# Kernel tuning notes

Measured on AMD Instinct MI355X. Metric: run time of the kernel, lower is better.

## Reference

```python
import jax, jax.numpy as jnp
import numpy as np

N = 50000
F = 128
E = 800000
HOP = 3
ALPHA = 0.2  # leaky relu slope


def setup_inputs() -> dict:
    key = jax.random.key(0)
    ks = jax.random.split(key, 6)
    x = jax.random.normal(ks[0], (N, F), dtype=jnp.float32)
    h0 = jax.random.normal(ks[1], (N, F), dtype=jnp.float32)
    edge_index = jax.random.randint(ks[2], (2, E), 0, N, dtype=jnp.int32)
    edge_weight = jax.random.uniform(ks[3], (E,), dtype=jnp.float32)
    # xavier-uniform-ish params
    lim_w = float(np.sqrt(6.0 / (F + F)))
    W_att = jax.random.uniform(ks[4], (F, F), dtype=jnp.float32, minval=-lim_w, maxval=lim_w)
    lim_a = 1.414 * float(np.sqrt(6.0 / (2 * F + 1)))
    a = jax.random.uniform(ks[5], (2 * F, 1), dtype=jnp.float32, minval=-lim_a, maxval=lim_a)
    temp = jnp.zeros((4,), dtype=jnp.float32)
    return {"x": x, "h0": h0, "edge_index": edge_index, "edge_weight": edge_weight,
            "W_att": W_att, "a": a, "temp": temp}


def _segment_softmax(e, rows, num_segments):
    m = jax.ops.segment_max(e, rows, num_segments=num_segments)
    m = jnp.where(jnp.isfinite(m), m, 0.0)  # guard empty rows
    ex = jnp.exp(e - m[rows])
    s = jax.ops.segment_sum(ex, rows, num_segments=num_segments)
    s = jnp.where(s > 0, s, 1.0)
    return ex / s[rows]


def reference(x, h0, edge_index, edge_weight, W_att, a, temp):
    rows, cols = edge_index[0], edge_index[1]
    # --- attention (edge-wise, never materializing dense NxN e) ---
    feat = x @ W_att                       # [N, F]
    f1 = (feat @ a[:F]).squeeze(-1)        # [N]
    f2 = (feat @ a[F:]).squeeze(-1)        # [N]
    e = f1[rows] + f2[cols]                # e[i,j] at edges
    e = jnp.where(e > 0, e, ALPHA * e)     # leaky relu
    att = _segment_softmax(e, rows, N)     # sparse row softmax values
    P = 0.5 * att
    # --- lifting bases ---
    coe = jax.nn.sigmoid(temp)
    rowsum = jax.ops.segment_sum(edge_weight * P, rows, num_segments=N)  # [N]
    update = x
    feat_prime = None
    for step in range(HOP):
        # sparse mm: U @ update
        update = jax.ops.segment_sum(att[:, None] * update[cols], rows, num_segments=N)
        feat_even = coe[0] * x + update
        feat_odd = update - feat_even * rowsum[:, None]
        feat_prime = feat_odd if step == 0 else coe[2] * feat_prime + (1.0 - coe[2]) * feat_odd
    return feat_prime
```

## Files before the change

### kernel.cpp

```cpp
#include <hip/hip_runtime.h>
#include <hip/hip_fp16.h>

#define NN 50000
#define FF 128
#define EE 800000
#define ALPHA 0.2f
#define ESHIFT 4.0f

#define NBINS 196
#define RPB 256
#define CAPB 5120
#define EPB 2048

__global__ void k_w(const float* __restrict__ W, const float* __restrict__ a,
                    float* __restrict__ w12) {
    int k = threadIdx.x;
    float s1 = 0.f, s2 = 0.f;
    const float* wr = W + k * FF;
    for (int j = 0; j < FF; ++j) {
        float w = wr[j];
        s1 += w * a[j];
        s2 += w * a[FF + j];
    }
    w12[k] = s1;
    w12[FF + k] = s2;
}

__global__ void k_f(const float* __restrict__ x, const float* __restrict__ w12,
                    float* __restrict__ f1, float* __restrict__ f2,
                    __half* __restrict__ xh) {
    int gid = blockIdx.x * blockDim.x + threadIdx.x;
    int node = gid >> 6;
    int lane = threadIdx.x & 63;
    if (node >= NN) return;
    float2 xv = ((const float2*)(x + (size_t)node * FF))[lane];
    ((__half2*)(xh + (size_t)node * FF))[lane] = __float22half2_rn(xv);
    float2 w1 = ((const float2*)w12)[lane];
    float2 w2 = ((const float2*)(w12 + FF))[lane];
    float s1 = xv.x * w1.x + xv.y * w1.y;
    float s2 = xv.x * w2.x + xv.y * w2.y;
#pragma unroll
    for (int o = 32; o > 0; o >>= 1) {
        s1 += __shfl_down(s1, o);
        s2 += __shfl_down(s2, o);
    }
    if (lane == 0) { f1[node] = s1; f2[node] = s2; }
}

__global__ void k_bin(const int* __restrict__ rows, const int* __restrict__ cols,
                      const float* __restrict__ ew, const float* __restrict__ f1,
                      const float* __restrict__ f2, int* __restrict__ bin_fill,
                      int2* __restrict__ binbuf) {
    __shared__ int cnt[NBINS];
    __shared__ int gbase[NBINS];
    int tid = threadIdx.x;
    if (tid < NBINS) cnt[tid] = 0;
    __syncthreads();
    int e0 = blockIdx.x * EPB;
    int rk[8], bn[8], rc[8], pay[8];
    bool vl[8];
#pragma unroll
    for (int k = 0; k < 8; ++k) {
        int e = e0 + k * 256 + tid;
        vl[k] = e < EE;
        if (vl[k]) {
            int r = rows[e], c = cols[e];
            float v = f1[r] + f2[c];
            v = v > 0.f ? v : ALPHA * v;
            float ex = __expf(v - ESHIFT);
            union { int i; __half2 h; } p;
            p.h = __floats2half2_rn(ex, ew[e] * ex);
            pay[k] = p.i;
            rc[k] = (r << 16) | c;
            bn[k] = r >> 8;
            rk[k] = atomicAdd(&cnt[bn[k]], 1);
        }
    }
    __syncthreads();
    if (tid < NBINS) {
        int c0 = cnt[tid];
        gbase[tid] = c0 ? atomicAdd(&bin_fill[tid], c0) : 0;
    }
    __syncthreads();
#pragma unroll
    for (int k = 0; k < 8; ++k) {
        if (vl[k]) {
            int pos = gbase[bn[k]] + rk[k];
            if (pos < CAPB) binbuf[(size_t)bn[k] * CAPB + pos] = make_int2(rc[k], pay[k]);
        }
    }
}

__global__ void k_csr(const int* __restrict__ bin_fill, const int2* __restrict__ binbuf,
                      int2* __restrict__ csr, int* __restrict__ row_ptr) {
    __shared__ int sc[256];
    __shared__ int lfill[RPB];
    __shared__ int2 grouped[CAPB];
    int tid = threadIdx.x;
    int bin = blockIdx.x;
    if (tid < 256) {
        int v = (tid < NBINS) ? bin_fill[tid] : 0;
        sc[tid] = v > CAPB ? CAPB : v;
    }
    __syncthreads();
    for (int s = 1; s < 256; s <<= 1) {
        int t = 0;
        if (tid < 256) t = sc[tid] + (tid >= s ? sc[tid - s] : 0);
        __syncthreads();
        if (tid < 256) sc[tid] = t;
        __syncthreads();
    }
    int base = (bin > 0) ? sc[bin - 1] : 0;
    int cnt = sc[bin] - base;
    __syncthreads();
    if (tid < RPB) lfill[tid] = 0;
    __syncthreads();
    int2 ent[5];
    int rnk[5], rl[5];
    bool vl[5];
#pragma unroll
    for (int it = 0; it < 5; ++it) {
        int i = tid + it * 1024;
        vl[it] = i < cnt;
        if (vl[it]) {
            ent[it] = binbuf[(size_t)bin * CAPB + i];
            rl[it] = (((unsigned)ent[it].x) >> 16) & 0xFF;
            rnk[it] = atomicAdd(&lfill[rl[it]], 1);
        }
    }
    __syncthreads();
    if (tid < 256) sc[tid] = lfill[tid];
    __syncthreads();
    for (int s = 1; s < 256; s <<= 1) {
        int t = 0;
        if (tid < 256) t = sc[tid] + (tid >= s ? sc[tid - s] : 0);
        __syncthreads();
        if (tid < 256) sc[tid] = t;
        __syncthreads();
    }
#pragma unroll
    for (int it = 0; it < 5; ++it) {
        if (vl[it])
            grouped[sc[rl[it]] - lfill[rl[it]] + rnk[it]] =
                make_int2(ent[it].x & 0xFFFF, ent[it].y);
    }
    __syncthreads();
    for (int i = tid; i < cnt; i += 1024) csr[base + i] = grouped[i];
    int r0 = bin << 8;
    int nrows = NN - r0 < RPB ? NN - r0 : RPB;
    if (tid < nrows) row_ptr[r0 + tid] = base + sc[tid] - lfill[tid];
    if (bin == NBINS - 1 && tid == 0) row_ptr[NN] = base + cnt;
}

__global__ void k_hop(const float* __restrict__ x, const __half* __restrict__ uin,
                      __half* __restrict__ uout, const int* __restrict__ row_ptr,
                      const int2* __restrict__ csr, const float* __restrict__ temp,
                      __half* __restrict__ S, float* __restrict__ out, int step) {
    int wave = threadIdx.x >> 6;
    int lane = threadIdx.x & 63;
    int r = __builtin_amdgcn_readfirstlane(blockIdx.x * 4 + wave);
    if (r >= NN) return;
    int beg = row_ptr[r], end = row_ptr[r + 1];
    const int2* bk = csr + beg;
    int d = end - beg;
    float ax = 0.f, ay = 0.f, se = 0.f, sw = 0.f;
    int j = 0;
    for (; j + 8 <= d; j += 8) {
        int2 b[8];
        __half2 h[8];
#pragma unroll
        for (int t = 0; t < 8; ++t) b[t] = bk[j + t];
#pragma unroll
        for (int t = 0; t < 8; ++t)
            h[t] = ((const __half2*)(uin + (size_t)b[t].x * FF))[lane];
#pragma unroll
        for (int t = 0; t < 8; ++t) {
            union { int i; __half2 h2; } p;
            p.i = b[t].y;
            float2 ee = __half22float2(p.h2);
            float2 u = __half22float2(h[t]);
            ax += ee.x * u.x;
            ay += ee.x * u.y;
            se += ee.x;
            sw += ee.y;
        }
    }
    for (; j < d; ++j) {
        int2 b = bk[j];
        __half2 hv = ((const __half2*)(uin + (size_t)b.x * FF))[lane];
        union { int i; __half2 h2; } p;
        p.i = b.y;
        float2 ee = __half22float2(p.h2);
        float2 u = __half22float2(hv);
        ax += ee.x * u.x;
        ay += ee.x * u.y;
        se += ee.x;
        sw += ee.y;
    }
    float inv = se > 0.f ? 1.f / se : 0.f;
    ax *= inv;
    ay *= inv;
    float c2 = 1.f / (1.f + __expf(-temp[2]));
    __half2* Sr = (__half2*)(S + (size_t)r * FF);
    if (step == 0) {
        ((__half2*)(uout + (size_t)r * FF))[lane] = __float22half2_rn(make_float2(ax, ay));
        float w0 = c2 * c2;
        Sr[lane] = __float22half2_rn(make_float2(w0 * ax, w0 * ay));
    } else if (step == 1) {
        ((__half2*)(uout + (size_t)r * FF))[lane] = __float22half2_rn(make_float2(ax, ay));
        float w1 = c2 * (1.f - c2);
        float2 sv = __half22float2(Sr[lane]);
        Sr[lane] = __float22half2_rn(make_float2(sv.x + w1 * ax, sv.y + w1 * ay));
    } else {
        float rs = 0.5f * sw * inv;
        float coe0 = 1.f / (1.f + __expf(-temp[0]));
        float w2 = 1.f - c2;
        float2 sv = __half22float2(Sr[lane]);
        float2 xv = ((const float2*)(x + (size_t)r * FF))[lane];
        float k1 = 1.f - rs;
        float k2 = coe0 * rs;
        ((float2*)(out + (size_t)r * FF))[lane] =
            make_float2(k1 * (sv.x + w2 * ax) - k2 * xv.x,
                        k1 * (sv.y + w2 * ay) - k2 * xv.y);
    }
}

extern "C" void kernel_launch(void* const* d_in, const int* in_sizes, int n_in,
                              void* d_out, int out_size, void* d_ws, size_t ws_size,
                              hipStream_t stream) {
    const float* x = (const float*)d_in[0];
    const int* eidx = (const int*)d_in[2];
    const int* rows = eidx;
    const int* cols = eidx + EE;
    const float* ew = (const float*)d_in[3];
    const float* W = (const float*)d_in[4];
    const float* a = (const float*)d_in[5];
    const float* temp = (const float*)d_in[6];
    float* out = (float*)d_out;

    float* ws = (float*)d_ws;
    int* bin_fill = (int*)ws;
    float* w12 = ws + 256;
    float* f1 = ws + 512;
    float* f2 = f1 + NN;
    int* row_ptr = (int*)(f2 + NN);
    int2* csr = (int2*)(row_ptr + NN + 64);
    __half* xh = (__half*)(csr + EE);
    __half* uh0 = xh + (size_t)NN * FF;
    __half* Sb = uh0 + (size_t)NN * FF;
    int2* binbuf = (int2*)Sb;
    __half* uh1 = xh;

    hipMemsetAsync(bin_fill, 0, NBINS * sizeof(int), stream);

    k_w<<<1, 128, 0, stream>>>(W, a, w12);
    k_f<<<(NN + 3) / 4, 256, 0, stream>>>(x, w12, f1, f2, xh);
    k_bin<<<(EE + EPB - 1) / EPB, 256, 0, stream>>>(rows, cols, ew, f1, f2, bin_fill, binbuf);
    k_csr<<<NBINS, 1024, 0, stream>>>(bin_fill, binbuf, csr, row_ptr);
    k_hop<<<(NN + 3) / 4, 256, 0, stream>>>(x, xh, uh0, row_ptr, csr, temp, Sb, out, 0);
    k_hop<<<(NN + 3) / 4, 256, 0, stream>>>(x, uh0, uh1, row_ptr, csr, temp, Sb, out, 1);
    k_hop<<<(NN + 3) / 4, 256, 0, stream>>>(x, uh1, nullptr, row_ptr, csr, temp, Sb, out, 2);
}
```

Before: 258.4 us.

## Split CSR build into 64-row windows with padded rows and half-wave edge gathers

The CSR build now runs as 784 blocks of 256 threads. Each block handles a quarter of a bin (64 rows) and scatters edges through per-row atomic cursors into a fixed-capacity window. It replaces the global scan plus shared-memory regroup over 1024-thread blocks. Each row's edge count is padded to an even number with a zero dummy edge, and rows are described by (begin, padded degree) pairs. In the hop kernel each half-wave processes alternate edges with 8-byte loads of four halves per lane, and the halves are combined with a cross-lane shuffle, so two neighbour rows are gathered at once. The aim is more parallelism in the CSR kernel and more memory-level parallelism in the gather, at the cost of padding and windows that can overflow if a 64-row group exceeds its capacity.

Measured after the change: 487.5 us. 1.89x slower.

```diff
diff --git a/kernel.cpp b/kernel.cpp
--- a/kernel.cpp
+++ b/kernel.cpp
@@ -8,9 +8,10 @@
 #define ESHIFT 4.0f
 
 #define NBINS 196
-#define RPB 256
 #define CAPB 5120
 #define EPB 2048
+#define NWIN 784
+#define WCAP 1600
 
 __global__ void k_w(const float* __restrict__ W, const float* __restrict__ a,
                     float* __restrict__ w12) {
@@ -92,136 +93,180 @@
 }
 
 __global__ void k_csr(const int* __restrict__ bin_fill, const int2* __restrict__ binbuf,
-                      int2* __restrict__ csr, int* __restrict__ row_ptr) {
-    __shared__ int sc[256];
-    __shared__ int lfill[RPB];
-    __shared__ int2 grouped[CAPB];
+                      int2* __restrict__ csr, int2* __restrict__ rowinfo) {
+    __shared__ int lfill[64];
+    __shared__ int pbase[65];
+    __shared__ int cursor[64];
     int tid = threadIdx.x;
-    int bin = blockIdx.x;
-    if (tid < 256) {
-        int v = (tid < NBINS) ? bin_fill[tid] : 0;
-        sc[tid] = v > CAPB ? CAPB : v;
-    }
-    __syncthreads();
-    for (int s = 1; s < 256; s <<= 1) {
-        int t = 0;
-        if (tid < 256) t = sc[tid] + (tid >= s ? sc[tid - s] : 0);
-        __syncthreads();
-        if (tid < 256) sc[tid] = t;
-        __syncthreads();
-    }
-    int base = (bin > 0) ? sc[bin - 1] : 0;
-    int cnt = sc[bin] - base;
-    __syncthreads();
-    if (tid < RPB) lfill[tid] = 0;
-    __syncthreads();
-    int2 ent[5];
-    int rnk[5], rl[5];
-    bool vl[5];
-#pragma unroll
-    for (int it = 0; it < 5; ++it) {
-        int i = tid + it * 1024;
-        vl[it] = i < cnt;
-        if (vl[it]) {
-            ent[it] = binbuf[(size_t)bin * CAPB + i];
-            rl[it] = (((unsigned)ent[it].x) >> 16) & 0xFF;
-            rnk[it] = atomicAdd(&lfill[rl[it]], 1);
-        }
-    }
-    __syncthreads();
-    if (tid < 256) sc[tid] = lfill[tid];
-    __syncthreads();
-    for (int s = 1; s < 256; s <<= 1) {
-        int t = 0;
-        if (tid < 256) t = sc[tid] + (tid >= s ? sc[tid - s] : 0);
-        __syncthreads();
-        if (tid < 256) sc[tid] = t;
-        __syncthreads();
-    }
-#pragma unroll
-    for (int it = 0; it < 5; ++it) {
-        if (vl[it])
-            grouped[sc[rl[it]] - lfill[rl[it]] + rnk[it]] =
-                make_int2(ent[it].x & 0xFFFF, ent[it].y);
-    }
-    __syncthreads();
-    for (int i = tid; i < cnt; i += 1024) csr[base + i] = grouped[i];
-    int r0 = bin << 8;
-    int nrows = NN - r0 < RPB ? NN - r0 : RPB;
-    if (tid < nrows) row_ptr[r0 + tid] = base + sc[tid] - lfill[tid];
-    if (bin == NBINS - 1 && tid == 0) row_ptr[NN] = base + cnt;
+    int w = blockIdx.x;
+    int bin = w >> 2, q = w & 3;
+    int cnt = bin_fill[bin];
+    if (cnt > CAPB) cnt = CAPB;
+    if (tid < 64) lfill[tid] = 0;
+    __syncthreads();
+    const int2* bb = binbuf + (size_t)bin * CAPB;
+    for (int i = tid; i < cnt; i += 256) {
+        int rl = (bb[i].x >> 16) & 0xFF;
+        if ((rl >> 6) == q) atomicAdd(&lfill[rl & 63], 1);
+    }
+    __syncthreads();
+    if (tid < 64) {
+        int pc = (lfill[tid] + 1) & ~1;
+        int s = pc;
+#pragma unroll
+        for (int o = 1; o < 64; o <<= 1) {
+            int t = __shfl_up(s, o);
+            if (tid >= o) s += t;
+        }
+        pbase[tid + 1] = s;
+        if (tid == 0) pbase[0] = 0;
+    }
+    __syncthreads();
+    int wbase = w * WCAP;
+    if (tid < 64) cursor[tid] = wbase + pbase[tid];
+    __syncthreads();
+    for (int i = tid; i < cnt; i += 256) {
+        int2 e = bb[i];
+        int rl = (e.x >> 16) & 0xFF;
+        if ((rl >> 6) == q) {
+            int p = atomicAdd(&cursor[rl & 63], 1);
+            csr[p] = make_int2(e.x & 0xFFFF, e.y);
+        }
+    }
+    __syncthreads();
+    if (tid < 64) {
+        int r = (bin << 8) + (q << 6) + tid;
+        if (r < NN) {
+            int beg = wbase + pbase[tid];
+            int dreal = lfill[tid];
+            int dpad = (dreal + 1) & ~1;
+            if (dreal & 1) csr[beg + dreal] = make_int2(0, 0);
+            rowinfo[r] = make_int2(beg, dpad);
+        }
+    }
+}
+
+__device__ __forceinline__ uint2 pack4(float a0, float a1, float a2, float a3) {
+    union { unsigned u; __half2 h; } p, q;
+    p.h = __floats2half2_rn(a0, a1);
+    q.h = __floats2half2_rn(a2, a3);
+    return make_uint2(p.u, q.u);
 }
 
 __global__ void k_hop(const float* __restrict__ x, const __half* __restrict__ uin,
-                      __half* __restrict__ uout, const int* __restrict__ row_ptr,
+                      __half* __restrict__ uout, const int2* __restrict__ rowinfo,
                       const int2* __restrict__ csr, const float* __restrict__ temp,
                       __half* __restrict__ S, float* __restrict__ out, int step) {
     int wave = threadIdx.x >> 6;
     int lane = threadIdx.x & 63;
     int r = __builtin_amdgcn_readfirstlane(blockIdx.x * 4 + wave);
     if (r >= NN) return;
-    int beg = row_ptr[r], end = row_ptr[r + 1];
-    const int2* bk = csr + beg;
-    int d = end - beg;
-    float ax = 0.f, ay = 0.f, se = 0.f, sw = 0.f;
+    int2 ri = rowinfo[r];
+    const int2* bk = csr + ri.x;
+    int d = ri.y;
+    int half = lane >> 5, fl = lane & 31;
+    float a0 = 0.f, a1 = 0.f, a2 = 0.f, a3 = 0.f, se = 0.f, sw = 0.f;
     int j = 0;
     for (; j + 8 <= d; j += 8) {
         int2 b[8];
-        __half2 h[8];
 #pragma unroll
         for (int t = 0; t < 8; ++t) b[t] = bk[j + t];
-#pragma unroll
-        for (int t = 0; t < 8; ++t)
-            h[t] = ((const __half2*)(uin + (size_t)b[t].x * FF))[lane];
-#pragma unroll
-        for (int t = 0; t < 8; ++t) {
-            union { int i; __half2 h2; } p;
-            p.i = b[t].y;
-            float2 ee = __half22float2(p.h2);
-            float2 u = __half22float2(h[t]);
-            ax += ee.x * u.x;
-            ay += ee.x * u.y;
+        uint2 uv[4];
+#pragma unroll
+        for (int t = 0; t < 4; ++t) {
+            int col = half ? b[2 * t + 1].x : b[2 * t].x;
+            uv[t] = *(const uint2*)(uin + (size_t)col * FF + fl * 4);
+        }
+#pragma unroll
+        for (int t = 0; t < 4; ++t) {
+            union { int i; __half2 h; } p;
+            p.i = half ? b[2 * t + 1].y : b[2 * t].y;
+            float2 ee = __half22float2(p.h);
+            union { unsigned u; __half2 h; } w0, w1;
+            w0.u = uv[t].x;
+            w1.u = uv[t].y;
+            float2 f01 = __half22float2(w0.h);
+            float2 f23 = __half22float2(w1.h);
+            a0 += ee.x * f01.x;
+            a1 += ee.x * f01.y;
+            a2 += ee.x * f23.x;
+            a3 += ee.x * f23.y;
             se += ee.x;
             sw += ee.y;
         }
     }
-    for (; j < d; ++j) {
-        int2 b = bk[j];
-        __half2 hv = ((const __half2*)(uin + (size_t)b.x * FF))[lane];
-        union { int i; __half2 h2; } p;
-        p.i = b.y;
-        float2 ee = __half22float2(p.h2);
-        float2 u = __half22float2(hv);
-        ax += ee.x * u.x;
-        ay += ee.x * u.y;
+    for (; j < d; j += 2) {
+        int2 b0 = bk[j], b1 = bk[j + 1];
+        union { int i; __half2 h; } p;
+        p.i = half ? b1.y : b0.y;
+        int col = half ? b1.x : b0.x;
+        uint2 uvt = *(const uint2*)(uin + (size_t)col * FF + fl * 4);
+        float2 ee = __half22float2(p.h);
+        union { unsigned u; __half2 h; } w0, w1;
+        w0.u = uvt.x;
+        w1.u = uvt.y;
+        float2 f01 = __half22float2(w0.h);
+        float2 f23 = __half22float2(w1.h);
+        a0 += ee.x * f01.x;
+        a1 += ee.x * f01.y;
+        a2 += ee.x * f23.x;
+        a3 += ee.x * f23.y;
         se += ee.x;
         sw += ee.y;
     }
+    se += __shfl_xor(se, 32);
+    sw += __shfl_xor(sw, 32);
+    a0 += __shfl_xor(a0, 32);
+    a1 += __shfl_xor(a1, 32);
+    a2 += __shfl_xor(a2, 32);
+    a3 += __shfl_xor(a3, 32);
     float inv = se > 0.f ? 1.f / se : 0.f;
-    ax *= inv;
-    ay *= inv;
+    a0 *= inv; a1 *= inv; a2 *= inv; a3 *= inv;
     float c2 = 1.f / (1.f + __expf(-temp[2]));
-    __half2* Sr = (__half2*)(S + (size_t)r * FF);
+    uint2* Srow = (uint2*)(S + (size_t)r * FF);
+    uint2* Urow = (uint2*)(uout + (size_t)r * FF);
     if (step == 0) {
-        ((__half2*)(uout + (size_t)r * FF))[lane] = __float22half2_rn(make_float2(ax, ay));
-        float w0 = c2 * c2;
-        Sr[lane] = __float22half2_rn(make_float2(w0 * ax, w0 * ay));
+        if (half == 0) {
+            Urow[fl] = pack4(a0, a1, a2, a3);
+        } else {
+            float w0c = c2 * c2;
+            Srow[fl] = pack4(w0c * a0, w0c * a1, w0c * a2, w0c * a3);
+        }
     } else if (step == 1) {
-        ((__half2*)(uout + (size_t)r * FF))[lane] = __float22half2_rn(make_float2(ax, ay));
-        float w1 = c2 * (1.f - c2);
-        float2 sv = __half22float2(Sr[lane]);
-        Sr[lane] = __float22half2_rn(make_float2(sv.x + w1 * ax, sv.y + w1 * ay));
+        if (half == 0) {
+            Urow[fl] = pack4(a0, a1, a2, a3);
+        } else {
+            float w1c = c2 * (1.f - c2);
+            uint2 sv = Srow[fl];
+            union { unsigned u; __half2 h; } s0, s1;
+            s0.u = sv.x;
+            s1.u = sv.y;
+            float2 v01 = __half22float2(s0.h);
+            float2 v23 = __half22float2(s1.h);
+            Srow[fl] = pack4(v01.x + w1c * a0, v01.y + w1c * a1,
+                             v23.x + w1c * a2, v23.y + w1c * a3);
+        }
     } else {
-        float rs = 0.5f * sw * inv;
-        float coe0 = 1.f / (1.f + __expf(-temp[0]));
-        float w2 = 1.f - c2;
-        float2 sv = __half22float2(Sr[lane]);
-        float2 xv = ((const float2*)(x + (size_t)r * FF))[lane];
-        float k1 = 1.f - rs;
-        float k2 = coe0 * rs;
-        ((float2*)(out + (size_t)r * FF))[lane] =
-            make_float2(k1 * (sv.x + w2 * ax) - k2 * xv.x,
-                        k1 * (sv.y + w2 * ay) - k2 * xv.y);
+        if (half == 0) {
+            float rs = 0.5f * sw * inv;
+            float coe0 = 1.f / (1.f + __expf(-temp[0]));
+            float w2c = 1.f - c2;
+            uint2 sv = Srow[fl];
+            union { unsigned u; __half2 h; } s0, s1;
+            s0.u = sv.x;
+            s1.u = sv.y;
+            float2 v01 = __half22float2(s0.h);
+            float2 v23 = __half22float2(s1.h);
+            float4 xv = ((const float4*)(x + (size_t)r * FF))[fl];
+            float k1 = 1.f - rs;
+            float k2 = coe0 * rs;
+            float4 o;
+            o.x = k1 * (v01.x + w2c * a0) - k2 * xv.x;
+            o.y = k1 * (v01.y + w2c * a1) - k2 * xv.y;
+            o.z = k1 * (v23.x + w2c * a2) - k2 * xv.z;
+            o.w = k1 * (v23.y + w2c * a3) - k2 * xv.w;
+            ((float4*)(out + (size_t)r * FF))[fl] = o;
+        }
     }
 }
 
@@ -243,9 +288,9 @@
     float* w12 = ws + 256;
     float* f1 = ws + 512;
     float* f2 = f1 + NN;
-    int* row_ptr = (int*)(f2 + NN);
-    int2* csr = (int2*)(row_ptr + NN + 64);
-    __half* xh = (__half*)(csr + EE);
+    int2* rowinfo = (int2*)(f2 + NN);
+    int2* csr = rowinfo + NN;
+    __half* xh = (__half*)(csr + (size_t)NWIN * WCAP);
     __half* uh0 = xh + (size_t)NN * FF;
     __half* Sb = uh0 + (size_t)NN * FF;
     int2* binbuf = (int2*)Sb;
@@ -256,8 +301,8 @@
     k_w<<<1, 128, 0, stream>>>(W, a, w12);
     k_f<<<(NN + 3) / 4, 256, 0, stream>>>(x, w12, f1, f2, xh);
     k_bin<<<(EE + EPB - 1) / EPB, 256, 0, stream>>>(rows, cols, ew, f1, f2, bin_fill, binbuf);
-    k_csr<<<NBINS, 1024, 0, stream>>>(bin_fill, binbuf, csr, row_ptr);
-    k_hop<<<(NN + 3) / 4, 256, 0, stream>>>(x, xh, uh0, row_ptr, csr, temp, Sb, out, 0);
-    k_hop<<<(NN + 3) / 4, 256, 0, stream>>>(x, uh0, uh1, row_ptr, csr, temp, Sb, out, 1);
-    k_hop<<<(NN + 3) / 4, 256, 0, stream>>>(x, uh1, nullptr, row_ptr, csr, temp, Sb, out, 2);
-}
+    k_csr<<<NWIN, 256, 0, stream>>>(bin_fill, binbuf, csr, rowinfo);
+    k_hop<<<(NN + 3) / 4, 256, 0, stream>>>(x, xh, uh0, rowinfo, csr, temp, Sb, out, 0);
+    k_hop<<<(NN + 3) / 4, 256, 0, stream>>>(x, uh0, uh1, rowinfo, csr, temp, Sb, out, 1);
+    k_hop<<<(NN + 3) / 4, 256, 0, stream>>>(x, uh1, nullptr, rowinfo, csr, temp, Sb, out, 2);
+}
```
